# Optimization experiments

Measured on AMD Instinct MI355X. Metric: run time of the kernel, lower is better.

The kernel has to match this reference:

```python
import jax, jax.numpy as jnp
import numpy as np

# --- static forest structure: NT complete ternary trees of depth DEPTH ---
BR, DEPTH, NT = 3, 7, 64            # branching factor (=L), edge-levels, num trees
OFF = [(3 ** d - 1) // 2 for d in range(DEPTH + 2)]  # BFS level offsets within a tree
NPT = OFF[DEPTH + 1]                 # nodes per tree = 3280
DIM = NT * NPT                       # total nodes = 209920
C_DIM, NGEN, M_SYM = 8, 8, 128


def build_tree():
    """Returns pos, leaves, batch, roots, levels [(parent_idx, child_idx)], unique-parents per level."""
    base = (np.arange(NT) * NPT)[:, None]
    pos = np.zeros(DIM, dtype=np.int64)
    levels, upar = [], []
    for d in range(1, DEPTH + 1):
        loc = np.arange(OFF[d], OFF[d + 1])
        ch = (base + loc).ravel()                                 # children at depth d (tree-major)
        pa = (base + (OFF[d - 1] + (loc - OFF[d]) // BR)).ravel() # their parents
        pos[ch] = np.tile((loc - OFF[d]) % BR, NT)
        levels.append((pa, ch))
        upar.append((base + np.arange(OFF[d - 1], OFF[d])).ravel())  # unique parents of level d
    leaves = (base + np.arange(OFF[DEPTH], OFF[DEPTH + 1])).ravel()
    batch = np.repeat(np.arange(NT), NPT)
    roots = np.arange(NT) * NPT
    return pos, leaves, batch, roots, levels, upar


def setup_inputs() -> dict:
    key = jax.random.key(0)
    k1, k2, k3, k4, k5 = jax.random.split(key, 5)
    pos_np, leaves_np, batch_np, _, _, _ = build_tree()
    return {
        "lam_A": jax.random.uniform(k1, (C_DIM, C_DIM, BR, NGEN), dtype=jnp.float32),
        "lam_B": jax.random.uniform(k2, (C_DIM, M_SYM, NGEN), dtype=jnp.float32),
        "lam_Pi": jax.random.uniform(k3, (C_DIM, BR, NGEN), dtype=jnp.float32),
        "lam_SP": jax.random.uniform(k4, (BR, NGEN), dtype=jnp.float32),
        "x": jax.random.randint(k5, (DIM,), 0, M_SYM, dtype=jnp.int64),
        "pos": jnp.asarray(pos_np),
        "leaves": jnp.asarray(leaves_np),
        "batch": jnp.asarray(batch_np),
    }


def reference(lam_A, lam_B, lam_Pi, lam_SP, x, pos, leaves, batch):
    # ReversedUpwardDownward (mode='bu') of PosteriorHiddenTreeMarkovModel.
    A = jax.nn.softmax(lam_A, axis=0)   # (C,C,L,G): softmax over first state axis
    Bm = jax.nn.softmax(lam_B, axis=1)  # (C,M,G): softmax over symbols
    Pi = jax.nn.softmax(lam_Pi, axis=0) # (C,L,G)
    SP = jax.nn.softmax(lam_SP, axis=0) # (L,G)
    C, G = A.shape[0], A.shape[-1]
    _, _, _, roots, levels, upar = build_tree()  # static structure

    beta = jnp.zeros((DIM, C, G), lam_A.dtype)
    t_beta = jnp.zeros((DIM, C, G), lam_A.dtype)

    # --- leaves init ---
    Pi_leaves = Pi[:, pos[leaves]]            # (C,Nl,G)
    bl = jnp.transpose(Pi_leaves * Bm[:, x[leaves]], (1, 0, 2))  # (Nl,C,G)
    beta = beta.at[leaves].set(bl / bl.sum(1, keepdims=True))

    # --- upward pass (deepest level first) ---
    for (pa, ch), u in zip(reversed(levels), reversed(upar)):
        SP_ch = SP[pos[ch]][:, None, None, :]                 # (E,1,1,G)
        A_ch = jnp.transpose(A[:, :, pos[ch]], (2, 0, 1, 3))  # (E,C,C,G)
        tb = (SP_ch * A_ch * beta[ch][:, None]).sum(2)        # (E,C,G) sum over child state
        t_beta = t_beta.at[pa].add(tb)
        bu = t_beta[u] * jnp.transpose(Bm[:, x[u]], (1, 0, 2))
        beta = beta.at[u].set(bu / bu.sum(1, keepdims=True))

    # --- downward pass ---
    eps = jnp.zeros((DIM, C, G), lam_A.dtype)
    ell = jnp.zeros((DIM, G), lam_A.dtype)
    eps = eps.at[roots].set(beta[roots])
    for pa, ch in levels:
        SP_ch = SP[pos[ch]]                                   # (E,G)
        A_ch = jnp.transpose(A[:, :, pos[ch]], (2, 0, 1, 3))  # (E,C,C,G)
        trans = SP_ch[:, None, None, :] * A_ch
        ej = (eps[pa][:, :, None, :] * trans * beta[ch][:, None, :, :]
              / t_beta[pa][:, :, None, :])                    # (E,C,C,G) joint posterior
        eps = eps.at[ch].set(ej.sum(1))
        ell = ell.at[ch].add((ej * jnp.log(A_ch)).sum((1, 2))
                             + ej.sum((1, 2)) * jnp.log(SP_ch))
    ell = ell + (eps * jnp.transpose(Bm[:, x], (1, 0, 2))).sum(1)
    ell = ell.at[leaves].add((eps[leaves] * jnp.transpose(jnp.log(Pi_leaves), (1, 0, 2))).sum(1))
    return -jax.ops.segment_sum(ell, batch, num_segments=NT)  # (NT,G)
```

## Files before the change

kernel.cpp:

```cpp
#include <hip/hip_runtime.h>


namespace {

constexpr int kNPT = 3280;
constexpr int kST  = 68;
__device__ __constant__ int LO[6] = {0, 1, 4, 13, 40, 121};
__device__ __constant__ int P3[5] = {1, 3, 9, 27, 81};

constexpr int oA   = 0;
constexpr int oALA = 1536;
constexpr int oBm  = 3072;
constexpr int oPi  = 11264;
constexpr int oLPi = 11456;
constexpr int oSP  = 11648;
constexpr int oLSP = 11672;
constexpr int oEnd = 11712;
constexpr int kB3  = 64 * 27 * 64;

__device__ __forceinline__ void leaf_beta(const float* __restrict__ sPi,
                                          const float* __restrict__ pBm,
                                          int p, int xv, int g, float* b)
{
    float s = 0.f;
    #pragma unroll
    for (int c = 0; c < 8; ++c) {
        b[c] = sPi[(c * 3 + p) * 8 + g] * pBm[xv * 64 + c * 8 + g];
        s += b[c];
    }
    float ig = __builtin_amdgcn_rcpf(s);
    #pragma unroll
    for (int c = 0; c < 8; ++c) b[c] *= ig;
}

__global__ __launch_bounds__(256)
void k0_params(const float* __restrict__ lamA, const float* __restrict__ lamB,
               const float* __restrict__ lamPi, const float* __restrict__ lamSP,
               float* __restrict__ P)
{
    const int tid = threadIdx.x;
    __shared__ float rmax[256], rsum[256];

    for (int col = tid; col < 192; col += 256) {
        int j = col / 24; int rem = col - j * 24; int p = rem >> 3; int g = rem & 7;
        float v[8]; float mx = -1e30f;
        #pragma unroll
        for (int i = 0; i < 8; ++i) {
            v[i] = lamA[((i * 8 + j) * 3 + p) * 8 + g];
            mx = fmaxf(mx, v[i]);
        }
        float s = 0.f;
        #pragma unroll
        for (int i = 0; i < 8; ++i) { v[i] = expf(v[i] - mx); s += v[i]; }
        float inv = 1.f / s;
        #pragma unroll
        for (int i = 0; i < 8; ++i) {
            int idx = ((i * 8 + j) * 3 + p) * 8 + g;
            float sm = v[i] * inv;
            P[oA + idx]   = sm;
            P[oALA + idx] = sm * logf(sm);
        }
    }
    {
        int row = tid >> 2, part = tid & 3;
        int c = row >> 3, g = row & 7, m0 = part * 32;
        float mx = -1e30f;
        for (int mm = 0; mm < 32; ++mm)
            mx = fmaxf(mx, lamB[(c * 128 + m0 + mm) * 8 + g]);
        rmax[tid] = mx;
        __syncthreads();
        float m4 = fmaxf(fmaxf(rmax[row * 4], rmax[row * 4 + 1]),
                         fmaxf(rmax[row * 4 + 2], rmax[row * 4 + 3]));
        float s = 0.f;
        for (int mm = 0; mm < 32; ++mm)
            s += expf(lamB[(c * 128 + m0 + mm) * 8 + g] - m4);
        rsum[tid] = s;
        __syncthreads();
        float stot = rsum[row * 4] + rsum[row * 4 + 1] + rsum[row * 4 + 2] + rsum[row * 4 + 3];
        float inv = 1.f / stot;
        for (int mm = 0; mm < 32; ++mm) {
            P[oBm + (m0 + mm) * 64 + c * 8 + g] =
                expf(lamB[(c * 128 + m0 + mm) * 8 + g] - m4) * inv;
        }
    }
    for (int col = tid; col < 24; col += 256) {
        int p = col >> 3; int g = col & 7;
        float v[8]; float mx = -1e30f;
        #pragma unroll
        for (int c = 0; c < 8; ++c) {
            v[c] = lamPi[(c * 3 + p) * 8 + g];
            mx = fmaxf(mx, v[c]);
        }
        float s = 0.f;
        #pragma unroll
        for (int c = 0; c < 8; ++c) { v[c] = expf(v[c] - mx); s += v[c]; }
        float inv = 1.f / s;
        #pragma unroll
        for (int c = 0; c < 8; ++c) {
            int idx = (c * 3 + p) * 8 + g;
            float sm = v[c] * inv;
            P[oPi + idx]  = sm;
            P[oLPi + idx] = logf(sm);
        }
    }
    if (tid < 8) {
        int g = tid;
        float v0 = lamSP[g], v1 = lamSP[8 + g], v2 = lamSP[16 + g];
        float mx = fmaxf(v0, fmaxf(v1, v2));
        float e0 = expf(v0 - mx), e1 = expf(v1 - mx), e2 = expf(v2 - mx);
        float inv = 1.f / (e0 + e1 + e2);
        P[oSP + g]       = e0 * inv; P[oSP + 8 + g]  = e1 * inv; P[oSP + 16 + g] = e2 * inv;
        P[oLSP + g]      = logf(e0 * inv);
        P[oLSP + 8 + g]  = logf(e1 * inv);
        P[oLSP + 16 + g] = logf(e2 * inv);
    }
}

__global__ __launch_bounds__(256)
void k1_up(const float* __restrict__ P, const int* __restrict__ x,
           float* __restrict__ b3)
{
    const int tid = threadIdx.x, w = tid >> 6, lane = tid & 63;
    const int n = lane >> 3, g = lane & 7;
    __shared__ float sA[1536], sPi[192], sSP[24];
    __shared__ float bW[4][40 * kST];
    __shared__ int   xW[4][124];
    for (int i = tid; i < 1536; i += 256) sA[i] = P[oA + i];
    for (int i = tid; i < 192; i += 256)  sPi[i] = P[oPi + i];
    if (tid < 24) sSP[tid] = P[oSP + tid];
    __syncthreads();
    const float* pBm = P + oBm;
    const int id = blockIdx.x * 4 + w, t = id / 27, q = id % 27, xb = t * kNPT;
    float* bw = bW[w]; int* xw = xW[w];

    for (int u = lane; u < 121; u += 64) {
        int gx;
        if (u == 0)       gx = 13 + q;
        else if (u < 4)   gx = 40  + q * 3  + (u - 1);
        else if (u < 13)  gx = 121 + q * 9  + (u - 4);
        else if (u < 40)  gx = 364 + q * 27 + (u - 13);
        else              gx = 1093 + q * 81 + (u - 40);
        xw[u] = x[xb + gx];
    }
    __builtin_amdgcn_wave_barrier();

    for (int e = 3; e >= 0; --e) {
        int cnt = P3[e];
        for (int base = 0; base < cnt; base += 8) {
            int pi = base + n;
            if (pi < cnt) {
                float acc[8];
                #pragma unroll
                for (int i = 0; i < 8; ++i) acc[i] = 0.f;
                #pragma unroll
                for (int k = 0; k < 3; ++k) {
                    float bj[8];
                    if (e == 3) {
                        leaf_beta(sPi, pBm, k, xw[40 + 3 * pi + k], g, bj);
                    } else {
                        int co = (LO[e + 1] + 3 * pi + k) * kST + g;
                        #pragma unroll
                        for (int j = 0; j < 8; ++j) bj[j] = bw[co + j * 8];
                    }
                    float spg = sSP[k * 8 + g];
                    #pragma unroll
                    for (int i = 0; i < 8; ++i) {
                        float s = 0.f;
                        #pragma unroll
                        for (int j = 0; j < 8; ++j)
                            s = fmaf(sA[((i * 8 + j) * 3 + k) * 8 + g], bj[j], s);
                        acc[i] = fmaf(spg, s, acc[i]);
                    }
                }
                int xv = xw[LO[e] + pi];
                float s = 0.f;
                #pragma unroll
                for (int i = 0; i < 8; ++i) { acc[i] *= pBm[xv * 64 + i * 8 + g]; s += acc[i]; }
                float ig = __builtin_amdgcn_rcpf(s);
                if (e == 0) {
                    #pragma unroll
                    for (int i = 0; i < 8; ++i) b3[id * 64 + i * 8 + g] = acc[i] * ig;
                } else {
                    int bo = (LO[e] + pi) * kST + g;
                    #pragma unroll
                    for (int i = 0; i < 8; ++i) bw[bo + i * 8] = acc[i] * ig;
                }
            }
        }
        __builtin_amdgcn_wave_barrier();
    }
}

__global__ __launch_bounds__(256)
void k2_mid(const float* __restrict__ P, const int* __restrict__ x,
            const float* __restrict__ b3, float* __restrict__ e3,
            float* __restrict__ out)
{
    const int tid = threadIdx.x, w = tid >> 6, lane = tid & 63;
    const int n = lane >> 3, g = lane & 7;
    __shared__ float sA[1536], sALA[1536], sSP[24], sLSP[24];
    __shared__ float b3W[4][27 * kST], bMW[4][13 * kST], sSW[4][13 * 8];
    __shared__ int   xW[4][40];
    for (int i = tid; i < 1536; i += 256) { sA[i] = P[oA + i]; sALA[i] = P[oALA + i]; }
    if (tid < 24) { sSP[tid] = P[oSP + tid]; sLSP[tid] = P[oLSP + tid]; }
    __syncthreads();
    const float* pBm = P + oBm;
    const int t = blockIdx.x * 4 + w, xb = t * kNPT;
    float* b3w = b3W[w]; float* bM = bMW[w]; float* sw = sSW[w]; int* xw = xW[w];

    for (int u = lane; u < 27 * 64; u += 64) {
        int slot = u >> 6, idx = u & 63;
        b3w[slot * kST + idx] = b3[(t * 27 + slot) * 64 + idx];
    }
    for (int u = lane; u < 40; u += 64) xw[u] = x[xb + u];
    __builtin_amdgcn_wave_barrier();

    for (int f = 2; f >= 0; --f) {
        int cnt = (f == 2) ? 9 : (f == 1 ? 3 : 1);
        int pl0 = (f == 2) ? 4 : (f == 1 ? 1 : 0);
        int cl0 = (f == 1) ? 4 : 1;
        for (int base = 0; base < cnt; base += 8) {
            int pi = base + n;
            if (pi < cnt) {
                float acc[8];
                #pragma unroll
                for (int i = 0; i < 8; ++i) acc[i] = 0.f;
                #pragma unroll
                for (int k = 0; k < 3; ++k) {
                    float bj[8];
                    if (f == 2) {
                        int co = (3 * pi + k) * kST + g;
                        #pragma unroll
                        for (int j = 0; j < 8; ++j) bj[j] = b3w[co + j * 8];
                    } else {
                        int co = (cl0 + 3 * pi + k) * kST + g;
                        #pragma unroll
                        for (int j = 0; j < 8; ++j) bj[j] = bM[co + j * 8];
                    }
                    float spg = sSP[k * 8 + g];
                    #pragma unroll
                    for (int i = 0; i < 8; ++i) {
                        float s = 0.f;
                        #pragma unroll
                        for (int j = 0; j < 8; ++j)
                            s = fmaf(sA[((i * 8 + j) * 3 + k) * 8 + g], bj[j], s);
                        acc[i] = fmaf(spg, s, acc[i]);
                    }
                }
                int slot = pl0 + pi;
                int xv = xw[slot];
                float s = 0.f;
                #pragma unroll
                for (int i = 0; i < 8; ++i) { acc[i] *= pBm[xv * 64 + i * 8 + g]; s += acc[i]; }
                sw[slot * 8 + g] = s;
                float ig = __builtin_amdgcn_rcpf(s);
                int bo = slot * kST + g;
                #pragma unroll
                for (int i = 0; i < 8; ++i) bM[bo + i * 8] = acc[i] * ig;
            }
        }
        __builtin_amdgcn_wave_barrier();
    }

    float ell = 0.f;
    if (n == 0) {
        int xv = xw[0];
        float invs = __builtin_amdgcn_rcpf(sw[g]);
        #pragma unroll
        for (int c = 0; c < 8; ++c)
            ell += bM[c * 8 + g] * pBm[xv * 64 + c * 8 + g];
        #pragma unroll
        for (int c = 0; c < 8; ++c)
            bM[c * 8 + g] = pBm[xv * 64 + c * 8 + g] * invs;
    }
    __builtin_amdgcn_wave_barrier();

    for (int f = 1; f <= 3; ++f) {
        int cnt = (f == 1) ? 3 : (f == 2 ? 9 : 27);
        int cl0 = (f == 1) ? 1 : (f == 2 ? 4 : 13);
        int pl0 = (f == 1) ? 0 : (f == 2 ? 1 : 4);
        for (int base = 0; base < cnt; base += 8) {
            int ci = base + n;
            if (ci < cnt) {
                int p = ci % 3;
                int ps = (pl0 + ci / 3) * kST + g;
                float r[8];
                #pragma unroll
                for (int i = 0; i < 8; ++i) r[i] = bM[ps + i * 8];
                float bj[8];
                if (f == 3) {
                    int co = ci * kST + g;
                    #pragma unroll
                    for (int j = 0; j < 8; ++j) bj[j] = b3w[co + j * 8];
                } else {
                    int co = (cl0 + ci) * kST + g;
                    #pragma unroll
                    for (int j = 0; j < 8; ++j) bj[j] = bM[co + j * 8];
                }
                float spg = sSP[p * 8 + g];
                float esum = 0.f, lg = 0.f;
                float ev[8];
                #pragma unroll
                for (int j = 0; j < 8; ++j) {
                    float s1 = 0.f, s2 = 0.f;
                    #pragma unroll
                    for (int i = 0; i < 8; ++i) {
                        int ai = ((i * 8 + j) * 3 + p) * 8 + g;
                        s1 = fmaf(r[i], sA[ai],   s1);
                        s2 = fmaf(r[i], sALA[ai], s2);
                    }
                    float bs = spg * bj[j];
                    ev[j] = bs * s1;
                    lg    = fmaf(bs, s2, lg);
                    esum += ev[j];
                }
                lg = fmaf(esum, sLSP[p * 8 + g], lg);
                int xv = xw[cl0 + ci];
                float Bmv[8];
                #pragma unroll
                for (int c = 0; c < 8; ++c) {
                    Bmv[c] = pBm[xv * 64 + c * 8 + g];
                    lg = fmaf(ev[c], Bmv[c], lg);
                }
                if (f == 3) {
                    #pragma unroll
                    for (int j = 0; j < 8; ++j)
                        e3[(t * 27 + ci) * 64 + j * 8 + g] = ev[j];
                } else {
                    float sv = sw[(cl0 + ci) * 8 + g];
                    int co = (cl0 + ci) * kST + g;
                    #pragma unroll
                    for (int j = 0; j < 8; ++j)
                        bM[co + j * 8] = ev[j] * Bmv[j] * __builtin_amdgcn_rcpf(bj[j] * sv);
                }
                ell += lg;
            }
        }
        __builtin_amdgcn_wave_barrier();
    }

    ell += __shfl_xor(ell, 8);
    ell += __shfl_xor(ell, 16);
    ell += __shfl_xor(ell, 32);
    if (n == 0) out[t * 8 + g] = -ell;
}

__global__ __launch_bounds__(256)
void k3_down(const float* __restrict__ P, const int* __restrict__ x,
             const float* __restrict__ e3, float* __restrict__ out)
{
    const int tid = threadIdx.x, w = tid >> 6, lane = tid & 63;
    const int n = lane >> 3, g = lane & 7;
    __shared__ float sA[1536], sALA[1536], sPi[192], sLPi[192], sSP[24], sLSP[24];
    __shared__ float bW[4][40 * kST];
    __shared__ float sSW[4][40 * 8];
    __shared__ int   xW[4][124];
    for (int i = tid; i < 1536; i += 256) { sA[i] = P[oA + i]; sALA[i] = P[oALA + i]; }
    for (int i = tid; i < 192; i += 256)  { sPi[i] = P[oPi + i]; sLPi[i] = P[oLPi + i]; }
    if (tid < 24) { sSP[tid] = P[oSP + tid]; sLSP[tid] = P[oLSP + tid]; }
    __syncthreads();
    const float* pBm = P + oBm;
    const int id = blockIdx.x * 4 + w, t = id / 27, q = id % 27, xb = t * kNPT;
    float* bw = bW[w]; float* sw = sSW[w]; int* xw = xW[w];

    for (int u = lane; u < 121; u += 64) {
        int gx;
        if (u == 0)       gx = 13 + q;
        else if (u < 4)   gx = 40  + q * 3  + (u - 1);
        else if (u < 13)  gx = 121 + q * 9  + (u - 4);
        else if (u < 40)  gx = 364 + q * 27 + (u - 13);
        else              gx = 1093 + q * 81 + (u - 40);
        xw[u] = x[xb + gx];
    }
    __builtin_amdgcn_wave_barrier();

    for (int e = 3; e >= 0; --e) {
        int cnt = P3[e];
        for (int base = 0; base < cnt; base += 8) {
            int pi = base + n;
            if (pi < cnt) {
                float acc[8];
                #pragma unroll
                for (int i = 0; i < 8; ++i) acc[i] = 0.f;
                #pragma unroll
                for (int k = 0; k < 3; ++k) {
                    float bj[8];
                    if (e == 3) {
                        leaf_beta(sPi, pBm, k, xw[40 + 3 * pi + k], g, bj);
                    } else {
                        int co = (LO[e + 1] + 3 * pi + k) * kST + g;
                        #pragma unroll
                        for (int j = 0; j < 8; ++j) bj[j] = bw[co + j * 8];
                    }
                    float spg = sSP[k * 8 + g];
                    #pragma unroll
                    for (int i = 0; i < 8; ++i) {
                        float s = 0.f;
                        #pragma unroll
                        for (int j = 0; j < 8; ++j)
                            s = fmaf(sA[((i * 8 + j) * 3 + k) * 8 + g], bj[j], s);
                        acc[i] = fmaf(spg, s, acc[i]);
                    }
                }
                if (e == 0) {
                    #pragma unroll
                    for (int i = 0; i < 8; ++i) bw[i * 8 + g] = acc[i];
                } else {
                    int slot = LO[e] + pi;
                    int xv = xw[slot];
                    float s = 0.f;
                    #pragma unroll
                    for (int i = 0; i < 8; ++i) { acc[i] *= pBm[xv * 64 + i * 8 + g]; s += acc[i]; }
                    sw[slot * 8 + g] = s;
                    float ig = __builtin_amdgcn_rcpf(s);
                    int bo = slot * kST + g;
                    #pragma unroll
                    for (int i = 0; i < 8; ++i) bw[bo + i * 8] = acc[i] * ig;
                }
            }
        }
        __builtin_amdgcn_wave_barrier();
    }

    bw[lane] = e3[id * 64 + lane] * __builtin_amdgcn_rcpf(bw[lane]);
    __builtin_amdgcn_wave_barrier();

    float ell = 0.f;
    for (int e = 1; e <= 4; ++e) {
        int cnt = P3[e], pl0 = LO[e - 1];
        for (int base = 0; base < cnt; base += 8) {
            int ci = base + n;
            if (ci < cnt) {
                int p = ci % 3;
                int ps = (pl0 + ci / 3) * kST + g;
                float r[8];
                #pragma unroll
                for (int i = 0; i < 8; ++i) r[i] = bw[ps + i * 8];
                float bj[8];
                int xv;
                if (e == 4) {
                    xv = xw[40 + ci];
                    leaf_beta(sPi, pBm, p, xv, g, bj);
                } else {
                    int slot = LO[e] + ci;
                    xv = xw[slot];
                    int co = slot * kST + g;
                    #pragma unroll
                    for (int j = 0; j < 8; ++j) bj[j] = bw[co + j * 8];
                }
                float spg = sSP[p * 8 + g];
                float esum = 0.f, lg = 0.f;
                float ev[8];
                #pragma unroll
                for (int j = 0; j < 8; ++j) {
                    float s1 = 0.f, s2 = 0.f;
                    #pragma unroll
                    for (int i = 0; i < 8; ++i) {
                        int ai = ((i * 8 + j) * 3 + p) * 8 + g;
                        s1 = fmaf(r[i], sA[ai],   s1);
                        s2 = fmaf(r[i], sALA[ai], s2);
                    }
                    float bs = spg * bj[j];
                    ev[j] = bs * s1;
                    lg    = fmaf(bs, s2, lg);
                    esum += ev[j];
                }
                lg = fmaf(esum, sLSP[p * 8 + g], lg);
                float Bmv[8];
                #pragma unroll
                for (int c = 0; c < 8; ++c) {
                    Bmv[c] = pBm[xv * 64 + c * 8 + g];
                    lg = fmaf(ev[c], Bmv[c], lg);
                }
                if (e < 4) {
                    int slot = LO[e] + ci;
                    float sv = sw[slot * 8 + g];
                    int co = slot * kST + g;
                    #pragma unroll
                    for (int j = 0; j < 8; ++j)
                        bw[co + j * 8] = ev[j] * Bmv[j] * __builtin_amdgcn_rcpf(bj[j] * sv);
                } else {
                    #pragma unroll
                    for (int c = 0; c < 8; ++c)
                        lg = fmaf(ev[c], sLPi[(c * 3 + p) * 8 + g], lg);
                }
                ell += lg;
            }
        }
        __builtin_amdgcn_wave_barrier();
    }

    ell += __shfl_xor(ell, 8);
    ell += __shfl_xor(ell, 16);
    ell += __shfl_xor(ell, 32);
    if (n == 0) atomicAdd(&out[t * 8 + g], -ell);
}

}

extern "C" void kernel_launch(void* const* d_in, const int* in_sizes, int n_in,
                              void* d_out, int out_size, void* d_ws, size_t ws_size,
                              hipStream_t stream) {
    const float* lamA  = (const float*)d_in[0];
    const float* lamB  = (const float*)d_in[1];
    const float* lamPi = (const float*)d_in[2];
    const float* lamSP = (const float*)d_in[3];
    const int*   x     = (const int*)d_in[4];
    float* out = (float*)d_out;
    float* P   = (float*)d_ws;
    float* b3  = P + oEnd;
    float* e3  = b3 + kB3;

    k0_params<<<dim3(1),   dim3(256), 0, stream>>>(lamA, lamB, lamPi, lamSP, P);
    k1_up    <<<dim3(432), dim3(256), 0, stream>>>(P, x, b3);
    k2_mid   <<<dim3(16),  dim3(256), 0, stream>>>(P, x, b3, e3, out);
    k3_down  <<<dim3(432), dim3(256), 0, stream>>>(P, x, e3, out);
}
```

Baseline: 167.0 us.

## Fuse four kernels into one persistent kernel with software grid barriers

Merges the parameter softmax, upward, middle and downward kernels into a single 432-block launch that synchronises through atomic-counter grid barriers. Each block now computes the small softmax tables into shared memory itself, so only the emission table goes through global memory, and the up-pass beta sums are kept in a padded shared row instead of being recomputed. This removes three launch gaps and a separate single-block parameter kernel. In exchange it relies on all 432 blocks being co-resident, has a magic-value reset handshake with a spin timeout, and serialises the middle stage onto a few waves while the other blocks wait.

```diff
diff --git a/kernel.cpp b/kernel.cpp
--- a/kernel.cpp
+++ b/kernel.cpp
@@ -4,19 +4,11 @@
 namespace {
 
 constexpr int kNPT = 3280;
-constexpr int kST  = 68;
+constexpr int kRS  = 72;
+constexpr unsigned kMAGIC = 0x13579BDFu;
+constexpr unsigned kNBLK  = 432;
 __device__ __constant__ int LO[6] = {0, 1, 4, 13, 40, 121};
 __device__ __constant__ int P3[5] = {1, 3, 9, 27, 81};
-
-constexpr int oA   = 0;
-constexpr int oALA = 1536;
-constexpr int oBm  = 3072;
-constexpr int oPi  = 11264;
-constexpr int oLPi = 11456;
-constexpr int oSP  = 11648;
-constexpr int oLSP = 11672;
-constexpr int oEnd = 11712;
-constexpr int kB3  = 64 * 27 * 64;
 
 __device__ __forceinline__ void leaf_beta(const float* __restrict__ sPi,
                                           const float* __restrict__ pBm,
@@ -33,20 +25,56 @@
     for (int c = 0; c < 8; ++c) b[c] *= ig;
 }
 
-__global__ __launch_bounds__(256)
-void k0_params(const float* __restrict__ lamA, const float* __restrict__ lamB,
-               const float* __restrict__ lamPi, const float* __restrict__ lamSP,
-               float* __restrict__ P)
+__device__ __forceinline__ void gbar(unsigned* c, int tid)
 {
-    const int tid = threadIdx.x;
-    __shared__ float rmax[256], rsum[256];
+    __syncthreads();
+    if (tid == 0) {
+        __threadfence();
+        atomicAdd(c, 1u);
+        unsigned long sp = 0;
+        while (__hip_atomic_load(c, __ATOMIC_ACQUIRE, __HIP_MEMORY_SCOPE_AGENT) < kNBLK) {
+            if (++sp > (1UL << 27)) break;
+            __builtin_amdgcn_s_sleep(2);
+        }
+        __threadfence();
+    }
+    __syncthreads();
+}
+
+__global__ __launch_bounds__(256, 2)
+void fused(const float* __restrict__ lamA, const float* __restrict__ lamB,
+           const float* __restrict__ lamPi, const float* __restrict__ lamSP,
+           const int* __restrict__ x, float* __restrict__ out,
+           unsigned* __restrict__ sync, float* __restrict__ bmG,
+           float* __restrict__ b3, float* __restrict__ e3)
+{
+    const int tid = threadIdx.x, w = tid >> 6, lane = tid & 63;
+    const int n = lane >> 3, g = lane & 7;
+    __shared__ float sA[1536], sALA[1536], sPi[192], sLPi[192], sSP[24], sLSP[24];
+    __shared__ float bW[4][40 * kRS];
+    __shared__ float bMid[13 * kRS];
+    __shared__ unsigned char xW[4][124];
+
+    if (tid == 0) {
+        if (blockIdx.x == 0) {
+            sync[1] = 0u; sync[2] = 0u; sync[3] = 0u;
+            __threadfence();
+            __hip_atomic_store(&sync[0], kMAGIC, __ATOMIC_RELEASE, __HIP_MEMORY_SCOPE_AGENT);
+        }
+        unsigned long sp = 0;
+        while (__hip_atomic_load(&sync[0], __ATOMIC_ACQUIRE, __HIP_MEMORY_SCOPE_AGENT) != kMAGIC) {
+            if (++sp > (1UL << 27)) break;
+            __builtin_amdgcn_s_sleep(2);
+        }
+    }
+    __syncthreads();
 
     for (int col = tid; col < 192; col += 256) {
-        int j = col / 24; int rem = col - j * 24; int p = rem >> 3; int g = rem & 7;
+        int j = col / 24; int rem = col - j * 24; int p = rem >> 3; int gg = rem & 7;
         float v[8]; float mx = -1e30f;
         #pragma unroll
         for (int i = 0; i < 8; ++i) {
-            v[i] = lamA[((i * 8 + j) * 3 + p) * 8 + g];
+            v[i] = lamA[((i * 8 + j) * 3 + p) * 8 + gg];
             mx = fmaxf(mx, v[i]);
         }
         float s = 0.f;
@@ -55,40 +83,18 @@
         float inv = 1.f / s;
         #pragma unroll
         for (int i = 0; i < 8; ++i) {
-            int idx = ((i * 8 + j) * 3 + p) * 8 + g;
+            int idx = ((i * 8 + j) * 3 + p) * 8 + gg;
             float sm = v[i] * inv;
-            P[oA + idx]   = sm;
-            P[oALA + idx] = sm * logf(sm);
-        }
-    }
-    {
-        int row = tid >> 2, part = tid & 3;
-        int c = row >> 3, g = row & 7, m0 = part * 32;
-        float mx = -1e30f;
-        for (int mm = 0; mm < 32; ++mm)
-            mx = fmaxf(mx, lamB[(c * 128 + m0 + mm) * 8 + g]);
-        rmax[tid] = mx;
-        __syncthreads();
-        float m4 = fmaxf(fmaxf(rmax[row * 4], rmax[row * 4 + 1]),
-                         fmaxf(rmax[row * 4 + 2], rmax[row * 4 + 3]));
-        float s = 0.f;
-        for (int mm = 0; mm < 32; ++mm)
-            s += expf(lamB[(c * 128 + m0 + mm) * 8 + g] - m4);
-        rsum[tid] = s;
-        __syncthreads();
-        float stot = rsum[row * 4] + rsum[row * 4 + 1] + rsum[row * 4 + 2] + rsum[row * 4 + 3];
-        float inv = 1.f / stot;
-        for (int mm = 0; mm < 32; ++mm) {
-            P[oBm + (m0 + mm) * 64 + c * 8 + g] =
-                expf(lamB[(c * 128 + m0 + mm) * 8 + g] - m4) * inv;
+            sA[idx]   = sm;
+            sALA[idx] = sm * logf(sm);
         }
     }
     for (int col = tid; col < 24; col += 256) {
-        int p = col >> 3; int g = col & 7;
+        int p = col >> 3; int gg = col & 7;
         float v[8]; float mx = -1e30f;
         #pragma unroll
         for (int c = 0; c < 8; ++c) {
-            v[c] = lamPi[(c * 3 + p) * 8 + g];
+            v[c] = lamPi[(c * 3 + p) * 8 + gg];
             mx = fmaxf(mx, v[c]);
         }
         float s = 0.f;
@@ -97,41 +103,54 @@
         float inv = 1.f / s;
         #pragma unroll
         for (int c = 0; c < 8; ++c) {
-            int idx = (c * 3 + p) * 8 + g;
+            int idx = (c * 3 + p) * 8 + gg;
             float sm = v[c] * inv;
-            P[oPi + idx]  = sm;
-            P[oLPi + idx] = logf(sm);
+            sPi[idx]  = sm;
+            sLPi[idx] = logf(sm);
         }
     }
     if (tid < 8) {
-        int g = tid;
-        float v0 = lamSP[g], v1 = lamSP[8 + g], v2 = lamSP[16 + g];
+        int gg = tid;
+        float v0 = lamSP[gg], v1 = lamSP[8 + gg], v2 = lamSP[16 + gg];
         float mx = fmaxf(v0, fmaxf(v1, v2));
         float e0 = expf(v0 - mx), e1 = expf(v1 - mx), e2 = expf(v2 - mx);
         float inv = 1.f / (e0 + e1 + e2);
-        P[oSP + g]       = e0 * inv; P[oSP + 8 + g]  = e1 * inv; P[oSP + 16 + g] = e2 * inv;
-        P[oLSP + g]      = logf(e0 * inv);
-        P[oLSP + 8 + g]  = logf(e1 * inv);
-        P[oLSP + 16 + g] = logf(e2 * inv);
-    }
-}
-
-__global__ __launch_bounds__(256)
-void k1_up(const float* __restrict__ P, const int* __restrict__ x,
-           float* __restrict__ b3)
-{
-    const int tid = threadIdx.x, w = tid >> 6, lane = tid & 63;
-    const int n = lane >> 3, g = lane & 7;
-    __shared__ float sA[1536], sPi[192], sSP[24];
-    __shared__ float bW[4][40 * kST];
-    __shared__ int   xW[4][124];
-    for (int i = tid; i < 1536; i += 256) sA[i] = P[oA + i];
-    for (int i = tid; i < 192; i += 256)  sPi[i] = P[oPi + i];
-    if (tid < 24) sSP[tid] = P[oSP + tid];
-    __syncthreads();
-    const float* pBm = P + oBm;
+        sSP[gg] = e0 * inv; sSP[8 + gg] = e1 * inv; sSP[16 + gg] = e2 * inv;
+        sLSP[gg] = logf(e0 * inv); sLSP[8 + gg] = logf(e1 * inv); sLSP[16 + gg] = logf(e2 * inv);
+    }
+    {
+        float* rr = &bW[0][0];
+        int row = tid >> 2, part = tid & 3;
+        int c = row >> 3, gg = row & 7, m0 = part * 32;
+        float mx = -1e30f;
+        if (blockIdx.x == 0)
+            for (int mm = 0; mm < 32; ++mm)
+                mx = fmaxf(mx, lamB[(c * 128 + m0 + mm) * 8 + gg]);
+        rr[tid] = mx;
+        __syncthreads();
+        float m4 = fmaxf(fmaxf(rr[row * 4], rr[row * 4 + 1]),
+                         fmaxf(rr[row * 4 + 2], rr[row * 4 + 3]));
+        float s = 0.f;
+        if (blockIdx.x == 0)
+            for (int mm = 0; mm < 32; ++mm)
+                s += expf(lamB[(c * 128 + m0 + mm) * 8 + gg] - m4);
+        rr[256 + tid] = s;
+        __syncthreads();
+        if (blockIdx.x == 0) {
+            float stot = rr[256 + row * 4] + rr[256 + row * 4 + 1]
+                       + rr[256 + row * 4 + 2] + rr[256 + row * 4 + 3];
+            float inv = 1.f / stot;
+            for (int mm = 0; mm < 32; ++mm)
+                bmG[(m0 + mm) * 64 + c * 8 + gg] =
+                    expf(lamB[(c * 128 + m0 + mm) * 8 + gg] - m4) * inv;
+        }
+    }
+    gbar(&sync[1], tid);
+
+    const float* pBm = bmG;
     const int id = blockIdx.x * 4 + w, t = id / 27, q = id % 27, xb = t * kNPT;
-    float* bw = bW[w]; int* xw = xW[w];
+    float* bw = &bW[w][0];
+    unsigned char* xw = &xW[w][0];
 
     for (int u = lane; u < 121; u += 64) {
         int gx;
@@ -140,7 +159,7 @@
         else if (u < 13)  gx = 121 + q * 9  + (u - 4);
         else if (u < 40)  gx = 364 + q * 27 + (u - 13);
         else              gx = 1093 + q * 81 + (u - 40);
-        xw[u] = x[xb + gx];
+        xw[u] = (unsigned char)x[xb + gx];
     }
     __builtin_amdgcn_wave_barrier();
 
@@ -158,7 +177,7 @@
                     if (e == 3) {
                         leaf_beta(sPi, pBm, k, xw[40 + 3 * pi + k], g, bj);
                     } else {
-                        int co = (LO[e + 1] + 3 * pi + k) * kST + g;
+                        int co = (LO[e + 1] + 3 * pi + k) * kRS + g;
                         #pragma unroll
                         for (int j = 0; j < 8; ++j) bj[j] = bw[co + j * 8];
                     }
@@ -172,255 +191,163 @@
                         acc[i] = fmaf(spg, s, acc[i]);
                     }
                 }
-                int xv = xw[LO[e] + pi];
-                float s = 0.f;
-                #pragma unroll
-                for (int i = 0; i < 8; ++i) { acc[i] *= pBm[xv * 64 + i * 8 + g]; s += acc[i]; }
-                float ig = __builtin_amdgcn_rcpf(s);
                 if (e == 0) {
                     #pragma unroll
+                    for (int i = 0; i < 8; ++i) bw[i * 8 + g] = acc[i];
+                    int xv = xw[0];
+                    float s = 0.f;
+                    #pragma unroll
+                    for (int i = 0; i < 8; ++i) { acc[i] *= pBm[xv * 64 + i * 8 + g]; s += acc[i]; }
+                    float ig = __builtin_amdgcn_rcpf(s);
+                    #pragma unroll
                     for (int i = 0; i < 8; ++i) b3[id * 64 + i * 8 + g] = acc[i] * ig;
-                } else {
-                    int bo = (LO[e] + pi) * kST + g;
-                    #pragma unroll
-                    for (int i = 0; i < 8; ++i) bw[bo + i * 8] = acc[i] * ig;
-                }
-            }
-        }
-        __builtin_amdgcn_wave_barrier();
-    }
-}
-
-__global__ __launch_bounds__(256)
-void k2_mid(const float* __restrict__ P, const int* __restrict__ x,
-            const float* __restrict__ b3, float* __restrict__ e3,
-            float* __restrict__ out)
-{
-    const int tid = threadIdx.x, w = tid >> 6, lane = tid & 63;
-    const int n = lane >> 3, g = lane & 7;
-    __shared__ float sA[1536], sALA[1536], sSP[24], sLSP[24];
-    __shared__ float b3W[4][27 * kST], bMW[4][13 * kST], sSW[4][13 * 8];
-    __shared__ int   xW[4][40];
-    for (int i = tid; i < 1536; i += 256) { sA[i] = P[oA + i]; sALA[i] = P[oALA + i]; }
-    if (tid < 24) { sSP[tid] = P[oSP + tid]; sLSP[tid] = P[oLSP + tid]; }
-    __syncthreads();
-    const float* pBm = P + oBm;
-    const int t = blockIdx.x * 4 + w, xb = t * kNPT;
-    float* b3w = b3W[w]; float* bM = bMW[w]; float* sw = sSW[w]; int* xw = xW[w];
-
-    for (int u = lane; u < 27 * 64; u += 64) {
-        int slot = u >> 6, idx = u & 63;
-        b3w[slot * kST + idx] = b3[(t * 27 + slot) * 64 + idx];
-    }
-    for (int u = lane; u < 40; u += 64) xw[u] = x[xb + u];
-    __builtin_amdgcn_wave_barrier();
-
-    for (int f = 2; f >= 0; --f) {
-        int cnt = (f == 2) ? 9 : (f == 1 ? 3 : 1);
-        int pl0 = (f == 2) ? 4 : (f == 1 ? 1 : 0);
-        int cl0 = (f == 1) ? 4 : 1;
-        for (int base = 0; base < cnt; base += 8) {
-            int pi = base + n;
-            if (pi < cnt) {
-                float acc[8];
-                #pragma unroll
-                for (int i = 0; i < 8; ++i) acc[i] = 0.f;
-                #pragma unroll
-                for (int k = 0; k < 3; ++k) {
-                    float bj[8];
-                    if (f == 2) {
-                        int co = (3 * pi + k) * kST + g;
-                        #pragma unroll
-                        for (int j = 0; j < 8; ++j) bj[j] = b3w[co + j * 8];
-                    } else {
-                        int co = (cl0 + 3 * pi + k) * kST + g;
-                        #pragma unroll
-                        for (int j = 0; j < 8; ++j) bj[j] = bM[co + j * 8];
-                    }
-                    float spg = sSP[k * 8 + g];
-                    #pragma unroll
-                    for (int i = 0; i < 8; ++i) {
-                        float s = 0.f;
-                        #pragma unroll
-                        for (int j = 0; j < 8; ++j)
-                            s = fmaf(sA[((i * 8 + j) * 3 + k) * 8 + g], bj[j], s);
-                        acc[i] = fmaf(spg, s, acc[i]);
-                    }
-                }
-                int slot = pl0 + pi;
-                int xv = xw[slot];
-                float s = 0.f;
-                #pragma unroll
-                for (int i = 0; i < 8; ++i) { acc[i] *= pBm[xv * 64 + i * 8 + g]; s += acc[i]; }
-                sw[slot * 8 + g] = s;
-                float ig = __builtin_amdgcn_rcpf(s);
-                int bo = slot * kST + g;
-                #pragma unroll
-                for (int i = 0; i < 8; ++i) bM[bo + i * 8] = acc[i] * ig;
-            }
-        }
-        __builtin_amdgcn_wave_barrier();
-    }
-
-    float ell = 0.f;
-    if (n == 0) {
-        int xv = xw[0];
-        float invs = __builtin_amdgcn_rcpf(sw[g]);
-        #pragma unroll
-        for (int c = 0; c < 8; ++c)
-            ell += bM[c * 8 + g] * pBm[xv * 64 + c * 8 + g];
-        #pragma unroll
-        for (int c = 0; c < 8; ++c)
-            bM[c * 8 + g] = pBm[xv * 64 + c * 8 + g] * invs;
-    }
-    __builtin_amdgcn_wave_barrier();
-
-    for (int f = 1; f <= 3; ++f) {
-        int cnt = (f == 1) ? 3 : (f == 2 ? 9 : 27);
-        int cl0 = (f == 1) ? 1 : (f == 2 ? 4 : 13);
-        int pl0 = (f == 1) ? 0 : (f == 2 ? 1 : 4);
-        for (int base = 0; base < cnt; base += 8) {
-            int ci = base + n;
-            if (ci < cnt) {
-                int p = ci % 3;
-                int ps = (pl0 + ci / 3) * kST + g;
-                float r[8];
-                #pragma unroll
-                for (int i = 0; i < 8; ++i) r[i] = bM[ps + i * 8];
-                float bj[8];
-                if (f == 3) {
-                    int co = ci * kST + g;
-                    #pragma unroll
-                    for (int j = 0; j < 8; ++j) bj[j] = b3w[co + j * 8];
-                } else {
-                    int co = (cl0 + ci) * kST + g;
-                    #pragma unroll
-                    for (int j = 0; j < 8; ++j) bj[j] = bM[co + j * 8];
-                }
-                float spg = sSP[p * 8 + g];
-                float esum = 0.f, lg = 0.f;
-                float ev[8];
-                #pragma unroll
-                for (int j = 0; j < 8; ++j) {
-                    float s1 = 0.f, s2 = 0.f;
-                    #pragma unroll
-                    for (int i = 0; i < 8; ++i) {
-                        int ai = ((i * 8 + j) * 3 + p) * 8 + g;
-                        s1 = fmaf(r[i], sA[ai],   s1);
-                        s2 = fmaf(r[i], sALA[ai], s2);
-                    }
-                    float bs = spg * bj[j];
-                    ev[j] = bs * s1;
-                    lg    = fmaf(bs, s2, lg);
-                    esum += ev[j];
-                }
-                lg = fmaf(esum, sLSP[p * 8 + g], lg);
-                int xv = xw[cl0 + ci];
-                float Bmv[8];
-                #pragma unroll
-                for (int c = 0; c < 8; ++c) {
-                    Bmv[c] = pBm[xv * 64 + c * 8 + g];
-                    lg = fmaf(ev[c], Bmv[c], lg);
-                }
-                if (f == 3) {
-                    #pragma unroll
-                    for (int j = 0; j < 8; ++j)
-                        e3[(t * 27 + ci) * 64 + j * 8 + g] = ev[j];
-                } else {
-                    float sv = sw[(cl0 + ci) * 8 + g];
-                    int co = (cl0 + ci) * kST + g;
-                    #pragma unroll
-                    for (int j = 0; j < 8; ++j)
-                        bM[co + j * 8] = ev[j] * Bmv[j] * __builtin_amdgcn_rcpf(bj[j] * sv);
-                }
-                ell += lg;
-            }
-        }
-        __builtin_amdgcn_wave_barrier();
-    }
-
-    ell += __shfl_xor(ell, 8);
-    ell += __shfl_xor(ell, 16);
-    ell += __shfl_xor(ell, 32);
-    if (n == 0) out[t * 8 + g] = -ell;
-}
-
-__global__ __launch_bounds__(256)
-void k3_down(const float* __restrict__ P, const int* __restrict__ x,
-             const float* __restrict__ e3, float* __restrict__ out)
-{
-    const int tid = threadIdx.x, w = tid >> 6, lane = tid & 63;
-    const int n = lane >> 3, g = lane & 7;
-    __shared__ float sA[1536], sALA[1536], sPi[192], sLPi[192], sSP[24], sLSP[24];
-    __shared__ float bW[4][40 * kST];
-    __shared__ float sSW[4][40 * 8];
-    __shared__ int   xW[4][124];
-    for (int i = tid; i < 1536; i += 256) { sA[i] = P[oA + i]; sALA[i] = P[oALA + i]; }
-    for (int i = tid; i < 192; i += 256)  { sPi[i] = P[oPi + i]; sLPi[i] = P[oLPi + i]; }
-    if (tid < 24) { sSP[tid] = P[oSP + tid]; sLSP[tid] = P[oLSP + tid]; }
-    __syncthreads();
-    const float* pBm = P + oBm;
-    const int id = blockIdx.x * 4 + w, t = id / 27, q = id % 27, xb = t * kNPT;
-    float* bw = bW[w]; float* sw = sSW[w]; int* xw = xW[w];
-
-    for (int u = lane; u < 121; u += 64) {
-        int gx;
-        if (u == 0)       gx = 13 + q;
-        else if (u < 4)   gx = 40  + q * 3  + (u - 1);
-        else if (u < 13)  gx = 121 + q * 9  + (u - 4);
-        else if (u < 40)  gx = 364 + q * 27 + (u - 13);
-        else              gx = 1093 + q * 81 + (u - 40);
-        xw[u] = x[xb + gx];
-    }
-    __builtin_amdgcn_wave_barrier();
-
-    for (int e = 3; e >= 0; --e) {
-        int cnt = P3[e];
-        for (int base = 0; base < cnt; base += 8) {
-            int pi = base + n;
-            if (pi < cnt) {
-                float acc[8];
-                #pragma unroll
-                for (int i = 0; i < 8; ++i) acc[i] = 0.f;
-                #pragma unroll
-                for (int k = 0; k < 3; ++k) {
-                    float bj[8];
-                    if (e == 3) {
-                        leaf_beta(sPi, pBm, k, xw[40 + 3 * pi + k], g, bj);
-                    } else {
-                        int co = (LO[e + 1] + 3 * pi + k) * kST + g;
-                        #pragma unroll
-                        for (int j = 0; j < 8; ++j) bj[j] = bw[co + j * 8];
-                    }
-                    float spg = sSP[k * 8 + g];
-                    #pragma unroll
-                    for (int i = 0; i < 8; ++i) {
-                        float s = 0.f;
-                        #pragma unroll
-                        for (int j = 0; j < 8; ++j)
-                            s = fmaf(sA[((i * 8 + j) * 3 + k) * 8 + g], bj[j], s);
-                        acc[i] = fmaf(spg, s, acc[i]);
-                    }
-                }
-                if (e == 0) {
-                    #pragma unroll
-                    for (int i = 0; i < 8; ++i) bw[i * 8 + g] = acc[i];
                 } else {
                     int slot = LO[e] + pi;
                     int xv = xw[slot];
                     float s = 0.f;
                     #pragma unroll
                     for (int i = 0; i < 8; ++i) { acc[i] *= pBm[xv * 64 + i * 8 + g]; s += acc[i]; }
-                    sw[slot * 8 + g] = s;
                     float ig = __builtin_amdgcn_rcpf(s);
-                    int bo = slot * kST + g;
+                    int bo = slot * kRS + g;
                     #pragma unroll
                     for (int i = 0; i < 8; ++i) bw[bo + i * 8] = acc[i] * ig;
+                    bw[slot * kRS + 64 + g] = s;
                 }
             }
         }
         __builtin_amdgcn_wave_barrier();
     }
+    gbar(&sync[2], tid);
+
+    if (q == 0) {
+        float ellm = 0.f;
+        for (int f = 2; f >= 0; --f) {
+            int cnt = (f == 2) ? 9 : (f == 1 ? 3 : 1);
+            int pl0 = (f == 2) ? 4 : (f == 1 ? 1 : 0);
+            int cl0 = (f == 1) ? 4 : 1;
+            for (int base = 0; base < cnt; base += 8) {
+                int pi = base + n;
+                if (pi < cnt) {
+                    float acc[8];
+                    #pragma unroll
+                    for (int i = 0; i < 8; ++i) acc[i] = 0.f;
+                    #pragma unroll
+                    for (int k = 0; k < 3; ++k) {
+                        float bj[8];
+                        if (f == 2) {
+                            const float* src = b3 + (t * 27 + 3 * pi + k) * 64 + g;
+                            #pragma unroll
+                            for (int j = 0; j < 8; ++j) bj[j] = src[j * 8];
+                        } else {
+                            int co = (cl0 + 3 * pi + k) * kRS + g;
+                            #pragma unroll
+                            for (int j = 0; j < 8; ++j) bj[j] = bMid[co + j * 8];
+                        }
+                        float spg = sSP[k * 8 + g];
+                        #pragma unroll
+                        for (int i = 0; i < 8; ++i) {
+                            float s = 0.f;
+                            #pragma unroll
+                            for (int j = 0; j < 8; ++j)
+                                s = fmaf(sA[((i * 8 + j) * 3 + k) * 8 + g], bj[j], s);
+                            acc[i] = fmaf(spg, s, acc[i]);
+                        }
+                    }
+                    int slot = pl0 + pi;
+                    int xv = x[xb + slot];
+                    float s = 0.f;
+                    #pragma unroll
+                    for (int i = 0; i < 8; ++i) { acc[i] *= pBm[xv * 64 + i * 8 + g]; s += acc[i]; }
+                    float ig = __builtin_amdgcn_rcpf(s);
+                    int bo = slot * kRS + g;
+                    #pragma unroll
+                    for (int i = 0; i < 8; ++i) bMid[bo + i * 8] = acc[i] * ig;
+                    bMid[slot * kRS + 64 + g] = s;
+                }
+            }
+            __builtin_amdgcn_wave_barrier();
+        }
+        if (n == 0) {
+            int xv = x[xb];
+            float invs = __builtin_amdgcn_rcpf(bMid[64 + g]);
+            #pragma unroll
+            for (int c = 0; c < 8; ++c)
+                ellm += bMid[c * 8 + g] * pBm[xv * 64 + c * 8 + g];
+            #pragma unroll
+            for (int c = 0; c < 8; ++c)
+                bMid[c * 8 + g] = pBm[xv * 64 + c * 8 + g] * invs;
+        }
+        __builtin_amdgcn_wave_barrier();
+        for (int f = 1; f <= 3; ++f) {
+            int cnt = (f == 1) ? 3 : (f == 2 ? 9 : 27);
+            int cl0 = (f == 1) ? 1 : (f == 2 ? 4 : 13);
+            int pl0 = (f == 1) ? 0 : (f == 2 ? 1 : 4);
+            for (int base = 0; base < cnt; base += 8) {
+                int ci = base + n;
+                if (ci < cnt) {
+                    int p = ci % 3;
+                    int ps = (pl0 + ci / 3) * kRS + g;
+                    float r[8];
+                    #pragma unroll
+                    for (int i = 0; i < 8; ++i) r[i] = bMid[ps + i * 8];
+                    float bj[8]; float sv = 0.f;
+                    if (f == 3) {
+                        const float* src = b3 + (t * 27 + ci) * 64 + g;
+                        #pragma unroll
+                        for (int j = 0; j < 8; ++j) bj[j] = src[j * 8];
+                    } else {
+                        int co = (cl0 + ci) * kRS + g;
+                        #pragma unroll
+                        for (int j = 0; j < 8; ++j) bj[j] = bMid[co + j * 8];
+                        sv = bMid[(cl0 + ci) * kRS + 64 + g];
+                    }
+                    float spg = sSP[p * 8 + g];
+                    float esum = 0.f, lg = 0.f;
+                    float ev[8];
+                    #pragma unroll
+                    for (int j = 0; j < 8; ++j) {
+                        float s1 = 0.f, s2 = 0.f;
+                        #pragma unroll
+                        for (int i = 0; i < 8; ++i) {
+                            int ai = ((i * 8 + j) * 3 + p) * 8 + g;
+                            s1 = fmaf(r[i], sA[ai],   s1);
+                            s2 = fmaf(r[i], sALA[ai], s2);
+                        }
+                        float bs = spg * bj[j];
+                        ev[j] = bs * s1;
+                        lg    = fmaf(bs, s2, lg);
+                        esum += ev[j];
+                    }
+                    lg = fmaf(esum, sLSP[p * 8 + g], lg);
+                    int xv = x[xb + cl0 + ci];
+                    float Bmv[8];
+                    #pragma unroll
+                    for (int c = 0; c < 8; ++c) {
+                        Bmv[c] = pBm[xv * 64 + c * 8 + g];
+                        lg = fmaf(ev[c], Bmv[c], lg);
+                    }
+                    if (f == 3) {
+                        #pragma unroll
+                        for (int j = 0; j < 8; ++j)
+                            e3[(t * 27 + ci) * 64 + j * 8 + g] = ev[j];
+                    } else {
+                        int co = (cl0 + ci) * kRS + g;
+                        #pragma unroll
+                        for (int j = 0; j < 8; ++j)
+                            bMid[co + j * 8] = ev[j] * Bmv[j]
+                                * __builtin_amdgcn_rcpf(bj[j] * sv);
+                    }
+                    ellm += lg;
+                }
+            }
+            __builtin_amdgcn_wave_barrier();
+        }
+        ellm += __shfl_xor(ellm, 8);
+        ellm += __shfl_xor(ellm, 16);
+        ellm += __shfl_xor(ellm, 32);
+        if (n == 0) out[t * 8 + g] = -ellm;
+    }
+    gbar(&sync[3], tid);
 
     bw[lane] = e3[id * 64 + lane] * __builtin_amdgcn_rcpf(bw[lane]);
     __builtin_amdgcn_wave_barrier();
@@ -432,11 +359,11 @@
             int ci = base + n;
             if (ci < cnt) {
                 int p = ci % 3;
-                int ps = (pl0 + ci / 3) * kST + g;
+                int ps = (pl0 + ci / 3) * kRS + g;
                 float r[8];
                 #pragma unroll
                 for (int i = 0; i < 8; ++i) r[i] = bw[ps + i * 8];
-                float bj[8];
+                float bj[8]; float sv = 0.f;
                 int xv;
                 if (e == 4) {
                     xv = xw[40 + ci];
@@ -444,9 +371,10 @@
                 } else {
                     int slot = LO[e] + ci;
                     xv = xw[slot];
-                    int co = slot * kST + g;
+                    int co = slot * kRS + g;
                     #pragma unroll
                     for (int j = 0; j < 8; ++j) bj[j] = bw[co + j * 8];
+                    sv = bw[slot * kRS + 64 + g];
                 }
                 float spg = sSP[p * 8 + g];
                 float esum = 0.f, lg = 0.f;
@@ -474,11 +402,11 @@
                 }
                 if (e < 4) {
                     int slot = LO[e] + ci;
-                    float sv = sw[slot * 8 + g];
-                    int co = slot * kST + g;
+                    int co = slot * kRS + g;
                     #pragma unroll
                     for (int j = 0; j < 8; ++j)
-                        bw[co + j * 8] = ev[j] * Bmv[j] * __builtin_amdgcn_rcpf(bj[j] * sv);
+                        bw[co + j * 8] = ev[j] * Bmv[j]
+                            * __builtin_amdgcn_rcpf(bj[j] * sv);
                 } else {
                     #pragma unroll
                     for (int c = 0; c < 8; ++c)
@@ -507,12 +435,11 @@
     const float* lamSP = (const float*)d_in[3];
     const int*   x     = (const int*)d_in[4];
     float* out = (float*)d_out;
-    float* P   = (float*)d_ws;
-    float* b3  = P + oEnd;
-    float* e3  = b3 + kB3;
-
-    k0_params<<<dim3(1),   dim3(256), 0, stream>>>(lamA, lamB, lamPi, lamSP, P);
-    k1_up    <<<dim3(432), dim3(256), 0, stream>>>(P, x, b3);
-    k2_mid   <<<dim3(16),  dim3(256), 0, stream>>>(P, x, b3, e3, out);
-    k3_down  <<<dim3(432), dim3(256), 0, stream>>>(P, x, e3, out);
+    unsigned* sync = (unsigned*)d_ws;
+    float* bmG = (float*)d_ws + 16;
+    float* b3  = bmG + 8192;
+    float* e3  = b3 + 1728 * 64;
+
+    fused<<<dim3(432), dim3(256), 0, stream>>>(
+        lamA, lamB, lamPi, lamSP, x, out, sync, bmG, b3, e3);
 }
```

After: 325.5 us. +94.9%, slower.
